# Kernel optimization log

Measured on AMD Instinct MI355X. Metric: run time of the kernel, lower is better.

The kernel has to match this reference:

```python
import jax, jax.numpy as jnp
import numpy as np

B, C = 16, 1024
EPS = 1e-12
TINY = 1e-9


def setup_inputs() -> dict:
    key = jax.random.key(0)
    k1, k2 = jax.random.split(key)
    lower = jax.random.normal(k1, (B, C), dtype=jnp.float32)
    # guarantee upper >= lower as required by bound propagation
    upper = lower + jax.random.uniform(k2, (B, C), dtype=jnp.float32)
    return {"lower": lower, "upper": upper}


def reference(lower, upper):
    l, u = lower, upper
    Bv, Cv = l.shape
    eye = jnp.eye(Cv, dtype=l.dtype)          # (C,C)
    offdiag = 1.0 - eye                        # zero on diagonal

    # pairwise logit differences d_ij = x_j - x_i, bounded by [l_d, u_d]; diag forced to 0
    l_d = (l[:, None, :] - u[:, :, None]) * offdiag   # (B,C,C)
    u_d = (u[:, None, :] - l[:, :, None]) * offdiag   # (B,C,C)

    exp_l = jnp.exp(l_d)
    exp_u = jnp.exp(u_d)

    # exp upper bound: secant over [l_d, u_d]
    denom = u_d - l_d
    a_u = (exp_u - exp_l) / (denom + EPS)
    a_u = jnp.where(jnp.abs(denom) < TINY, exp_u, a_u)
    b_u = exp_l - a_u * l_d

    # exp lower bound: tangent at midpoint t
    t = 0.5 * (l_d + u_d)
    a_l = jnp.exp(t)
    b_l = a_l - a_l * t                        # exp(t) - a_l * t

    # zero diagonal entries (i == j term excluded from the sum)
    a_u = a_u * offdiag
    b_u = b_u * offdiag
    a_l = a_l * offdiag
    b_l = b_l * offdiag
    exp_l_od = exp_l * offdiag
    exp_u_od = exp_u * offdiag

    S_l = exp_l_od.sum(axis=2)                 # (B,C)
    S_u = exp_u_od.sum(axis=2)                 # (B,C)

    # linear coefficients of S_i w.r.t. logits x: off-diag from a, diag collects -sum_j a_ij
    sum_a_u = a_u.sum(axis=2)                  # (B,C)
    sum_a_l = a_l.sum(axis=2)
    coef_S_upper = a_u - eye[None, :, :] * sum_a_u[:, :, None]
    coef_S_lower = a_l - eye[None, :, :] * sum_a_l[:, :, None]
    bias_S_upper = b_u.sum(axis=2)
    bias_S_lower = b_l.sum(axis=2)

    # g(S) = 1 / (1 + S), decreasing & convex
    g_at_S_l = 1.0 / (1.0 + S_l)
    g_at_S_u = 1.0 / (1.0 + S_u)

    # upper relaxation of g: tangent (secant of decreasing convex fn swaps roles)
    denom_g = S_u - S_l
    m_u = (g_at_S_u - g_at_S_l) / (denom_g + EPS)
    m_u = jnp.where(jnp.abs(denom_g) < TINY, -1.0 / (1.0 + S_u) ** 2, m_u)
    c_u = g_at_S_l - m_u * S_l

    # lower relaxation of g: tangent at S_u
    m_l = -1.0 / (1.0 + S_u) ** 2
    c_l = 1.0 / (1.0 + S_u) - m_l * S_u

    # compose (m_u >= ... careful with sign handled as in original: direct product)
    final_upper_coef = m_u[:, :, None] * coef_S_upper   # (B,C,C)
    final_lower_coef = m_l[:, :, None] * coef_S_lower   # (B,C,C)
    final_upper_bias = m_u * bias_S_upper + c_u          # (B,C)
    final_lower_bias = m_l * bias_S_lower + c_l          # (B,C)

    soft_lower = jnp.clip(g_at_S_u, 0.0, 1.0)
    soft_upper = jnp.clip(g_at_S_l, 0.0, 1.0)

    return (soft_lower, soft_upper,
            final_lower_coef, final_upper_coef,
            final_lower_bias, final_upper_bias)
```

## Files before the change

### kernel.cpp

```cpp
#include <hip/hip_runtime.h>

namespace {

constexpr int B = 16;
constexpr int C = 1024;
constexpr int BC = B * C;
constexpr long long BCC = (long long)B * C * C;
constexpr float EPS  = 1e-12f;
constexpr float TINY = 1e-9f;
constexpr int TI = 8;

using f32x4 = __attribute__((ext_vector_type(4))) float;

__global__ __launch_bounds__(256) void bounded_softmax_kernel(
    const float* __restrict__ lower,
    const float* __restrict__ upper,
    float* __restrict__ out)
{
    const int tid = threadIdx.x;
    constexpr int rowsPerBatch = C / TI;
    const int b  = blockIdx.x / rowsPerBatch;
    const int i0 = (blockIdx.x % rowsPerBatch) * TI;

    const float* __restrict__ lrow = lower + b * C;
    const float* __restrict__ urow = upper + b * C;

    const f32x4 lj4 = *reinterpret_cast<const f32x4*>(lrow + tid * 4);
    const f32x4 uj4 = *reinterpret_cast<const f32x4*>(urow + tid * 4);
    float lk[4], wk[4], El[4], Eu[4], Em[4];
    float s0 = 0.f, s1 = 0.f, s2 = 0.f, s3 = 0.f;
    #pragma unroll
    for (int k = 0; k < 4; ++k) {
        const float lj = lj4[k];
        const float uj = uj4[k];
        lk[k] = lj;
        wk[k] = uj - lj;
        El[k] = __expf(lj);
        Eu[k] = __expf(uj);
        const float mk = 0.5f * (lj + uj);
        Em[k] = __expf(mk);
        s0 += El[k]; s1 += Eu[k]; s2 += Em[k]; s3 += mk * Em[k];
    }

    __shared__ float red0[4][4];
    __shared__ float bs[4];
    __shared__ float red[2][4][2];
    const int lane = tid & 63;
    const int wid  = tid >> 6;
    #pragma unroll
    for (int o = 32; o > 0; o >>= 1) {
        s0 += __shfl_down(s0, o);
        s1 += __shfl_down(s1, o);
        s2 += __shfl_down(s2, o);
        s3 += __shfl_down(s3, o);
    }
    if (lane == 0) {
        red0[wid][0] = s0; red0[wid][1] = s1;
        red0[wid][2] = s2; red0[wid][3] = s3;
    }
    __syncthreads();
    if (tid < 4)
        bs[tid] = red0[0][tid] + red0[1][tid] + red0[2][tid] + red0[3][tid];
    __syncthreads();
    const float SEl = bs[0], SEu = bs[1], SEm = bs[2], SmEm = bs[3];

    for (int r = 0; r < TI; ++r) {
        const int i = i0 + r;
        const float l_i = lrow[i];
        const float u_i = urow[i];
        const float w_i = u_i - l_i;
        const float m_i = 0.5f * (l_i + u_i);
        const float e_li = __expf(-l_i);
        const float e_ui = __expf(-u_i);
        const float e_mi = __expf(-m_i);
        const float ewp  = __expf(w_i);
        const float ewn  = __expf(-w_i);

        const float S_l  = fmaf(e_ui, SEl, -ewn);
        const float S_u  = fmaf(e_li, SEu, -ewp);
        const float SA_l = fmaf(e_mi, SEm, -1.0f);
        const float SB_l = SA_l - e_mi * SmEm + m_i * e_mi * SEm;

        float au[4];
        float ra = 0.f, rb = 0.f;
        #pragma unroll
        for (int k = 0; k < 4; ++k) {
            const float eu    = Eu[k] * e_li;
            const float el    = El[k] * e_ui;
            const float denom = wk[k] + w_i;
            float a = (eu - el) * __builtin_amdgcn_rcpf(denom + EPS);
            a = (fabsf(denom) < TINY) ? eu : a;
            au[k] = a;
            const float l_d = lk[k] - u_i;
            ra += a;
            rb = fmaf(a, l_d, rb);
        }
        #pragma unroll
        for (int o = 32; o > 0; o >>= 1) {
            ra += __shfl_down(ra, o);
            rb += __shfl_down(rb, o);
        }
        const int p = r & 1;
        if (lane == 0) { red[p][wid][0] = ra; red[p][wid][1] = rb; }
        __syncthreads();
        const float sa_full = red[p][0][0] + red[p][1][0] + red[p][2][0] + red[p][3][0];
        const float sb_full = red[p][0][1] + red[p][1][1] + red[p][2][1] + red[p][3][1];

        const float dden = w_i + w_i;
        float a_d = (ewp - ewn) * __builtin_amdgcn_rcpf(dden + EPS);
        a_d = (fabsf(dden) < TINY) ? ewp : a_d;
        const float SA_u  = sa_full - a_d;
        const float SBu2  = sb_full + a_d * w_i;
        const float SB_u  = S_l - SBu2;

        const float g_l = 1.0f / (1.0f + S_l);
        const float g_u = 1.0f / (1.0f + S_u);
        const float dg  = S_u - S_l;
        float m_u = (g_u - g_l) / (dg + EPS);
        m_u = (fabsf(dg) < TINY) ? (-g_u * g_u) : m_u;
        const float c_u = g_l - m_u * S_l;
        const float m_l = -g_u * g_u;
        const float c_l = g_u - m_l * S_u;

        const int row = b * C + i;
        float* __restrict__ lower_coef = out + 2 * BC + (long long)row * C;
        float* __restrict__ upper_coef = out + 2 * BC + BCC + (long long)row * C;

        const float Kl = m_l * e_mi;
        const float dl = -m_l * SA_l;
        const float du = -m_u * SA_u;
        f32x4 lv, uv;
        #pragma unroll
        for (int k = 0; k < 4; ++k) {
            const int j = tid * 4 + k;
            lv[k] = (j == i) ? dl : Kl * Em[k];
            uv[k] = (j == i) ? du : m_u * au[k];
        }
        __builtin_nontemporal_store(lv, reinterpret_cast<f32x4*>(lower_coef + tid * 4));
        __builtin_nontemporal_store(uv, reinterpret_cast<f32x4*>(upper_coef + tid * 4));

        if (tid == 0) {
            out[row]                         = fminf(fmaxf(g_u, 0.f), 1.f);
            out[BC + row]                    = fminf(fmaxf(g_l, 0.f), 1.f);
            out[2 * BC + 2 * BCC + row]      = fmaf(m_l, SB_l, c_l);
            out[2 * BC + 2 * BCC + BC + row] = fmaf(m_u, SB_u, c_u);
        }
    }
}

}

extern "C" void kernel_launch(void* const* d_in, const int* in_sizes, int n_in,
                              void* d_out, int out_size, void* d_ws, size_t ws_size,
                              hipStream_t stream) {
    const float* lower = (const float*)d_in[0];
    const float* upper = (const float*)d_in[1];
    float* out = (float*)d_out;
    bounded_softmax_kernel<<<dim3(BC / TI), dim3(256), 0, stream>>>(lower, upper, out);
}
```

Baseline: 145.5 us.

## Assign one row per wavefront to remove per-row block barriers

Each wavefront now handles whole rows, two rows per wave, so the per-row reduction is a wave-level xor shuffle and needs no __syncthreads. Per-column exp values are staged in shared memory and read back per row. The second barrier in the initial reduction is also dropped. Nontemporal stores are replaced with regular vector stores, which may affect cache behaviour on this store-bound output.

```diff
diff --git a/kernel.cpp b/kernel.cpp
--- a/kernel.cpp
+++ b/kernel.cpp
@@ -17,7 +17,9 @@
     const float* __restrict__ upper,
     float* __restrict__ out)
 {
-    const int tid = threadIdx.x;
+    const int tid  = threadIdx.x;
+    const int lane = tid & 63;
+    const int wid  = tid >> 6;
     constexpr int rowsPerBatch = C / TI;
     const int b  = blockIdx.x / rowsPerBatch;
     const int i0 = (blockIdx.x % rowsPerBatch) * TI;
@@ -25,28 +27,28 @@
     const float* __restrict__ lrow = lower + b * C;
     const float* __restrict__ urow = upper + b * C;
 
+    __shared__ float sEl[C], sEu[C], sWk[C], sEm[C];
+    __shared__ float red0[4][4];
+
     const f32x4 lj4 = *reinterpret_cast<const f32x4*>(lrow + tid * 4);
     const f32x4 uj4 = *reinterpret_cast<const f32x4*>(urow + tid * 4);
-    float lk[4], wk[4], El[4], Eu[4], Em[4];
+    f32x4 tEl, tEu, tWk, tEm;
     float s0 = 0.f, s1 = 0.f, s2 = 0.f, s3 = 0.f;
     #pragma unroll
     for (int k = 0; k < 4; ++k) {
         const float lj = lj4[k];
         const float uj = uj4[k];
-        lk[k] = lj;
-        wk[k] = uj - lj;
-        El[k] = __expf(lj);
-        Eu[k] = __expf(uj);
+        const float El = __expf(lj);
+        const float Eu = __expf(uj);
         const float mk = 0.5f * (lj + uj);
-        Em[k] = __expf(mk);
-        s0 += El[k]; s1 += Eu[k]; s2 += Em[k]; s3 += mk * Em[k];
+        const float Em = __expf(mk);
+        tEl[k] = El; tEu[k] = Eu; tWk[k] = uj - lj; tEm[k] = Em;
+        s0 += El; s1 += Eu; s2 += Em; s3 += mk * Em;
     }
-
-    __shared__ float red0[4][4];
-    __shared__ float bs[4];
-    __shared__ float red[2][4][2];
-    const int lane = tid & 63;
-    const int wid  = tid >> 6;
+    *reinterpret_cast<f32x4*>(&sEl[tid * 4]) = tEl;
+    *reinterpret_cast<f32x4*>(&sEu[tid * 4]) = tEu;
+    *reinterpret_cast<f32x4*>(&sWk[tid * 4]) = tWk;
+    *reinterpret_cast<f32x4*>(&sEm[tid * 4]) = tEm;
     #pragma unroll
     for (int o = 32; o > 0; o >>= 1) {
         s0 += __shfl_down(s0, o);
@@ -59,13 +61,14 @@
         red0[wid][2] = s2; red0[wid][3] = s3;
     }
     __syncthreads();
-    if (tid < 4)
-        bs[tid] = red0[0][tid] + red0[1][tid] + red0[2][tid] + red0[3][tid];
-    __syncthreads();
-    const float SEl = bs[0], SEu = bs[1], SEm = bs[2], SmEm = bs[3];
+    const float SEl  = red0[0][0] + red0[1][0] + red0[2][0] + red0[3][0];
+    const float SEu  = red0[0][1] + red0[1][1] + red0[2][1] + red0[3][1];
+    const float SEm  = red0[0][2] + red0[1][2] + red0[2][2] + red0[3][2];
+    const float SmEm = red0[0][3] + red0[1][3] + red0[2][3] + red0[3][3];
 
-    for (int r = 0; r < TI; ++r) {
-        const int i = i0 + r;
+    #pragma unroll
+    for (int r = 0; r < 2; ++r) {
+        const int i = i0 + wid + 4 * r;
         const float l_i = lrow[i];
         const float u_i = urow[i];
         const float w_i = u_i - l_i;
@@ -76,42 +79,45 @@
         const float ewp  = __expf(w_i);
         const float ewn  = __expf(-w_i);
 
+        float a[16];
+        float ra = 0.f, rc = 0.f;
+        #pragma unroll
+        for (int q = 0; q < 4; ++q) {
+            const int jb = q * 256 + lane * 4;
+            const f32x4 El4 = *reinterpret_cast<const f32x4*>(&sEl[jb]);
+            const f32x4 Eu4 = *reinterpret_cast<const f32x4*>(&sEu[jb]);
+            const f32x4 Wk4 = *reinterpret_cast<const f32x4*>(&sWk[jb]);
+            const f32x4 Lj4 = *reinterpret_cast<const f32x4*>(lrow + jb);
+            #pragma unroll
+            for (int k = 0; k < 4; ++k) {
+                const float eu    = Eu4[k] * e_li;
+                const float el    = El4[k] * e_ui;
+                const float denom = Wk4[k] + w_i;
+                float av = (eu - el) * __builtin_amdgcn_rcpf(denom + EPS);
+                av = (fabsf(denom) < TINY) ? eu : av;
+                a[q * 4 + k] = av;
+                ra += av;
+                rc = fmaf(av, Lj4[k], rc);
+            }
+        }
+        #pragma unroll
+        for (int o = 1; o < 64; o <<= 1) {
+            ra += __shfl_xor(ra, o);
+            rc += __shfl_xor(rc, o);
+        }
+
         const float S_l  = fmaf(e_ui, SEl, -ewn);
         const float S_u  = fmaf(e_li, SEu, -ewp);
         const float SA_l = fmaf(e_mi, SEm, -1.0f);
         const float SB_l = SA_l - e_mi * SmEm + m_i * e_mi * SEm;
 
-        float au[4];
-        float ra = 0.f, rb = 0.f;
-        #pragma unroll
-        for (int k = 0; k < 4; ++k) {
-            const float eu    = Eu[k] * e_li;
-            const float el    = El[k] * e_ui;
-            const float denom = wk[k] + w_i;
-            float a = (eu - el) * __builtin_amdgcn_rcpf(denom + EPS);
-            a = (fabsf(denom) < TINY) ? eu : a;
-            au[k] = a;
-            const float l_d = lk[k] - u_i;
-            ra += a;
-            rb = fmaf(a, l_d, rb);
-        }
-        #pragma unroll
-        for (int o = 32; o > 0; o >>= 1) {
-            ra += __shfl_down(ra, o);
-            rb += __shfl_down(rb, o);
-        }
-        const int p = r & 1;
-        if (lane == 0) { red[p][wid][0] = ra; red[p][wid][1] = rb; }
-        __syncthreads();
-        const float sa_full = red[p][0][0] + red[p][1][0] + red[p][2][0] + red[p][3][0];
-        const float sb_full = red[p][0][1] + red[p][1][1] + red[p][2][1] + red[p][3][1];
-
         const float dden = w_i + w_i;
         float a_d = (ewp - ewn) * __builtin_amdgcn_rcpf(dden + EPS);
         a_d = (fabsf(dden) < TINY) ? ewp : a_d;
-        const float SA_u  = sa_full - a_d;
-        const float SBu2  = sb_full + a_d * w_i;
-        const float SB_u  = S_l - SBu2;
+        const float SA_u = ra - a_d;
+        const float rb_full = rc - u_i * ra;
+        const float SBu2 = rb_full + a_d * w_i;
+        const float SB_u = S_l - SBu2;
 
         const float g_l = 1.0f / (1.0f + S_l);
         const float g_u = 1.0f / (1.0f + S_u);
@@ -129,17 +135,22 @@
         const float Kl = m_l * e_mi;
         const float dl = -m_l * SA_l;
         const float du = -m_u * SA_u;
-        f32x4 lv, uv;
         #pragma unroll
-        for (int k = 0; k < 4; ++k) {
-            const int j = tid * 4 + k;
-            lv[k] = (j == i) ? dl : Kl * Em[k];
-            uv[k] = (j == i) ? du : m_u * au[k];
+        for (int q = 0; q < 4; ++q) {
+            const int jb = q * 256 + lane * 4;
+            const f32x4 Em4 = *reinterpret_cast<const f32x4*>(&sEm[jb]);
+            f32x4 lv, uv;
+            #pragma unroll
+            for (int k = 0; k < 4; ++k) {
+                const int j = jb + k;
+                lv[k] = (j == i) ? dl : Kl * Em4[k];
+                uv[k] = (j == i) ? du : m_u * a[q * 4 + k];
+            }
+            *reinterpret_cast<f32x4*>(lower_coef + jb) = lv;
+            *reinterpret_cast<f32x4*>(upper_coef + jb) = uv;
         }
-        __builtin_nontemporal_store(lv, reinterpret_cast<f32x4*>(lower_coef + tid * 4));
-        __builtin_nontemporal_store(uv, reinterpret_cast<f32x4*>(upper_coef + tid * 4));
 
-        if (tid == 0) {
+        if (lane == 0) {
             out[row]                         = fminf(fmaxf(g_u, 0.f), 1.f);
             out[BC + row]                    = fminf(fmaxf(g_l, 0.f), 1.f);
             out[2 * BC + 2 * BCC + row]      = fmaf(m_l, SB_l, c_l);
```

Measured after the change: 138.1 us. -5.1%, faster.
